# Kernel optimization log

Measured on AMD Instinct MI355X. Metric: run time of the kernel, lower is better.

The kernel has to match this reference:

```python
import jax, jax.numpy as jnp
import numpy as np

# Config constants (match init_kwargs / config)
B = 16        # config.BATCH_SIZE
T = 2048      # config.TRAIN_LEN
C = 256       # input channels (input_shape[-1])
K = 8         # kernel_size
F = 256       # nb_filters
DIL = 4       # dilation_rate


def setup_inputs() -> dict:
    key = jax.random.key(0)
    k1, k2, k3 = jax.random.split(key, 3)
    inputs = jax.random.normal(k1, (B, T, C), dtype=jnp.float32)
    kernel = jax.random.normal(k2, (C, K, F), dtype=jnp.float32) * 0.05
    bias = jax.random.normal(k3, (F,), dtype=jnp.float32) * 0.05
    return {"inputs": inputs, "kernel": kernel, "bias": bias}


def reference(inputs, kernel, bias):
    # Original TF layer computes, per (b,t,k,f):
    #   raw[b,t,k,f] = sum_c (x[b,t,c] * kernel[c,k,f] + bias[f])
    #               = conv[b,t,k,f] + C * bias[f]
    # (bias is added BEFORE the reduce_sum over the channel axis, so it is
    #  scaled by C — we reproduce that quirk faithfully.)
    # Then each (t,k) slice is scatter-added to output time t + k*dilation
    # (the gather_nd + zero-pad construction in TF implements exactly this
    #  dilated transposed-conv scatter; non-matching positions gather zeros),
    # and finally the last T timesteps are kept.
    Bq, Tq, Cq = inputs.shape
    Kq, Fq = kernel.shape[1], kernel.shape[2]
    conv = jnp.einsum('btc,ckf->btkf', inputs, kernel) + jnp.asarray(Cq, inputs.dtype) * bias
    L = Tq + (Kq - 1) * DIL  # final_time_len
    # scatter positions: out[i + j*DIL] += conv[:, i, j, :]
    pos = (jnp.arange(Tq)[:, None] + DIL * jnp.arange(Kq)[None, :]).reshape(-1)  # (T*K,)
    out = jnp.zeros((Bq, L, Fq), dtype=conv.dtype)
    out = out.at[:, pos, :].add(conv.reshape(Bq, Tq * Kq, Fq))
    return out[:, -Tq:, :]
```

## Files before the change

### kernel.cpp

```cpp
#include <hip/hip_runtime.h>
#include <hip/hip_bf16.h>


#define B_   16
#define T_   2048
#define C_   256
#define KT   8
#define F_   256
#define SH   28
#define BT   128
#define WIN  156
#define FB   19968
#define ABF  19968
#define ABFB 9984

typedef __attribute__((ext_vector_type(8))) short short8;
typedef __attribute__((ext_vector_type(4))) float floatx4;
typedef __attribute__((ext_vector_type(4))) int   intx4;

__device__ inline void gload16(const void* g, void* l) {
    __builtin_amdgcn_global_load_lds(
        (const __attribute__((address_space(1))) void*)g,
        (__attribute__((address_space(3))) void*)l, 16, 0, 0);
}

__device__ inline short8 cvt8(float4 a, float4 b) {
    float v[8] = {a.x, a.y, a.z, a.w, b.x, b.y, b.z, b.w};
    short8 r;
    #pragma unroll
    for (int i = 0; i < 8; ++i) {
        __hip_bfloat16 h = __float2bfloat16(v[i]);
        r[i] = *reinterpret_cast<const short*>(&h);
    }
    return r;
}

__global__ __launch_bounds__(256) void wprep_kernel(const float* __restrict__ W,
                                                    ushort* __restrict__ Wf) {
    const int tid  = threadIdx.x;
    const int fid  = blockIdx.x * 4 + (tid >> 6);
    const int lane = tid & 63;
    const int g    = fid & 15;
    const int S    = fid >> 4;
    const int j    = S & 7, c = S >> 3;
    const int c0   = c * 32 + (lane >> 4) * 8;
    const int f    = g * 16 + (lane & 15);
    short8 pk;
    #pragma unroll
    for (int i = 0; i < 8; ++i) {
        __hip_bfloat16 h = __float2bfloat16(W[((c0 + i) * KT + j) * F_ + f]);
        pk[i] = *reinterpret_cast<const short*>(&h);
    }
    *reinterpret_cast<short8*>(Wf + (size_t)fid * 512 + lane * 8) = pk;
}

__global__ __launch_bounds__(256, 2) void deconv_kernel(
        const float* __restrict__ x, const ushort* __restrict__ Wf,
        const float* __restrict__ bias, float* __restrict__ out) {
    __shared__ alignas(16) char smem[39936];
    const int bid = blockIdx.x;
    const int fh  = bid & 1;
    const int tb  = bid >> 1;
    const int b   = tb & 15;
    const int t0  = (tb >> 4) * BT;
    const int tid = threadIdx.x;
    const int w   = tid >> 6, lane = tid & 63;
    const int l16 = lane & 15, q = lane >> 4;
    const int wm  = w >> 1, wf2 = w & 1;
    const char* wfbase = (const char*)Wf +
        (size_t)(fh * 8 + wf2 * 4) * 1024 + (size_t)lane * 16;

#define VMW(N_) do { asm volatile("s_waitcnt vmcnt(" #N_ ")" ::: "memory"); \
        __builtin_amdgcn_sched_barrier(0); } while (0)
#define LKW() do { asm volatile("s_waitcnt lgkmcnt(0)" ::: "memory");       \
        __builtin_amdgcn_sched_barrier(0); } while (0)
#define BAR() do { __builtin_amdgcn_sched_barrier(0);                       \
        __builtin_amdgcn_s_barrier();                                       \
        asm volatile("" ::: "memory");                                      \
        __builtin_amdgcn_sched_barrier(0); } while (0)

#define A_ROUND(k_, cc_) do {                                               \
        const int u_ = (k_) * 256 + tid;                                    \
        if ((k_) < 4 || tid < 224) {                                        \
            const int row_ = u_ >> 3, s_ = u_ & 7;                          \
            const int v_   = (s_ + 8 - (row_ & 7)) & 7;                     \
            int tr_ = t0 + row_; if (tr_ > T_ - 1) tr_ = T_ - 1;            \
            gload16(x + ((size_t)(b * T_ + tr_) * C_ + (cc_) * 32 + v_ * 4),\
                    smem + ((k_) * 256 + w * 64) * 16);                     \
        } } while (0)

#define B_ISSUE(S_, sl_) do {                                               \
        const char* p_ = wfbase + (size_t)(S_) * 16384;                     \
        asm volatile("global_load_dwordx4 %0, %1, off"                      \
            : "=v"(bR[sl_][0]) : "v"(p_) : "memory");                       \
        asm volatile("global_load_dwordx4 %0, %1, off offset:1024"          \
            : "=v"(bR[sl_][1]) : "v"(p_) : "memory");                       \
        asm volatile("global_load_dwordx4 %0, %1, off offset:2048"          \
            : "=v"(bR[sl_][2]) : "v"(p_) : "memory");                       \
        asm volatile("global_load_dwordx4 %0, %1, off offset:3072"          \
            : "=v"(bR[sl_][3]) : "v"(p_) : "memory");                       \
        } while (0)

#define CVT_ROUND(r_, par_) do {                                            \
        if ((r_) < 2 || tid < 112) {                                        \
            const int task_ = (r_) * 256 + tid;                             \
            const int row_ = task_ >> 2, g_ = task_ & 3;                    \
            const int s1_ = (2 * g_ + row_) & 7;                            \
            const int s2_ = (2 * g_ + 1 + row_) & 7;                        \
            float4 u0_ = *(const float4*)(smem + (row_ * 8 + s1_) * 16);    \
            float4 u1_ = *(const float4*)(smem + (row_ * 8 + s2_) * 16);    \
            short8 pk_ = {0,0,0,0,0,0,0,0};                                 \
            if (t0 + row_ < T_) pk_ = cvt8(u0_, u1_);                       \
            const int p_ = g_ ^ ((row_ >> 1) & 3);                          \
            *(short8*)(smem + ABF + (par_) * ABFB + (row_ * 4 + p_) * 16)   \
                = pk_;                                                      \
        } } while (0)

#define LOAD_A(buf_, j_, arr) do {                                          \
        const char* ab_ = smem + ABF + (buf_) * ABFB;                       \
        _Pragma("unroll")                                                   \
        for (int mf = 0; mf < 4; ++mf) {                                    \
            const int row_ = wm * 64 + (SH - 4 * (j_)) + mf * 16 + l16;     \
            const int p_   = q ^ ((row_ >> 1) & 3);                         \
            arr[mf] = *(const short8*)(ab_ + (row_ * 4 + p_) * 16);         \
        } } while (0)

#define MFMA_TAP(arr, slot_) do {                                           \
        __builtin_amdgcn_s_setprio(1);                                      \
        _Pragma("unroll")                                                   \
        for (int mf = 0; mf < 4; ++mf)                                      \
            _Pragma("unroll")                                               \
            for (int nf = 0; nf < 4; ++nf)                                  \
                acc[mf][nf] = __builtin_amdgcn_mfma_f32_16x16x32_bf16(      \
                    arr[mf], *(short8*)&bR[slot_][nf],                      \
                    acc[mf][nf], 0, 0, 0);                                  \
        __builtin_amdgcn_s_setprio(0);                                      \
        } while (0)

#define CHUNK(c_) do {                                                      \
        LOAD_A((c_) & 1, 0, a0);                                            \
        A_ROUND(0, (c_)+1); A_ROUND(1, (c_)+1); A_ROUND(2, (c_)+1);         \
        A_ROUND(3, (c_)+1); A_ROUND(4, (c_)+1);                             \
        LOAD_A((c_) & 1, 1, a1);                                            \
        B_ISSUE((c_)*8+2, (((c_)*8+2)%3)); VMW(13);                         \
        MFMA_TAP(a0, (((c_)*8+0)%3));                                       \
        LOAD_A((c_) & 1, 2, a0);                                            \
        B_ISSUE((c_)*8+3, (((c_)*8+3)%3)); VMW(13);                         \
        MFMA_TAP(a1, (((c_)*8+1)%3));                                       \
        LOAD_A((c_) & 1, 3, a1);                                            \
        B_ISSUE((c_)*8+4, (((c_)*8+4)%3)); VMW(8);                          \
        MFMA_TAP(a0, (((c_)*8+2)%3));                                       \
        BAR();                                                              \
        LOAD_A((c_) & 1, 4, a0);                                            \
        B_ISSUE((c_)*8+5, (((c_)*8+5)%3)); VMW(8);                          \
        MFMA_TAP(a1, (((c_)*8+3)%3));                                       \
        LOAD_A((c_) & 1, 5, a1);                                            \
        CVT_ROUND(0, ((c_)+1)&1);                                           \
        B_ISSUE((c_)*8+6, (((c_)*8+6)%3)); VMW(8);                          \
        MFMA_TAP(a0, (((c_)*8+4)%3));                                       \
        LOAD_A((c_) & 1, 6, a0);                                            \
        CVT_ROUND(1, ((c_)+1)&1);                                           \
        B_ISSUE((c_)*8+7, (((c_)*8+7)%3)); VMW(8);                          \
        MFMA_TAP(a1, (((c_)*8+5)%3));                                       \
        LOAD_A((c_) & 1, 7, a1);                                            \
        CVT_ROUND(2, ((c_)+1)&1);                                           \
        B_ISSUE((c_)*8+8, (((c_)*8+8)%3)); VMW(8);                          \
        MFMA_TAP(a0, (((c_)*8+6)%3));                                       \
        B_ISSUE((c_)*8+9, (((c_)*8+9)%3)); VMW(8);                          \
        MFMA_TAP(a1, (((c_)*8+7)%3));                                       \
        LKW(); BAR();                                                       \
        } while (0)

    float bf4[4];
    #pragma unroll
    for (int nf = 0; nf < 4; ++nf)
        bf4[nf] = bias[fh * 128 + wf2 * 64 + nf * 16 + l16];

    floatx4 acc[4][4];
    #pragma unroll
    for (int mf = 0; mf < 4; ++mf)
        #pragma unroll
        for (int nf = 0; nf < 4; ++nf)
            acc[mf][nf] = (floatx4){0.f, 0.f, 0.f, 0.f};

    short8 a0[4], a1[4];
    intx4  bR[3][4];

    A_ROUND(0, 0); A_ROUND(1, 0); A_ROUND(2, 0); A_ROUND(3, 0); A_ROUND(4, 0);
    B_ISSUE(0, 0); B_ISSUE(1, 1);
    VMW(8);
    BAR();
    CVT_ROUND(0, 0); CVT_ROUND(1, 0); CVT_ROUND(2, 0);
    LKW(); BAR();

    CHUNK(0); CHUNK(1); CHUNK(2); CHUNK(3);
    CHUNK(4); CHUNK(5); CHUNK(6);

    LOAD_A(1, 0, a0);
    LOAD_A(1, 1, a1);
    B_ISSUE(58, 1); VMW(8); MFMA_TAP(a0, 2); LOAD_A(1, 2, a0);
    B_ISSUE(59, 2); VMW(8); MFMA_TAP(a1, 0); LOAD_A(1, 3, a1);
    B_ISSUE(60, 0); VMW(8); MFMA_TAP(a0, 1); LOAD_A(1, 4, a0);
    B_ISSUE(61, 1); VMW(8); MFMA_TAP(a1, 2); LOAD_A(1, 5, a1);
    B_ISSUE(62, 2); VMW(8); MFMA_TAP(a0, 0); LOAD_A(1, 6, a0);
    B_ISSUE(63, 0); VMW(8); MFMA_TAP(a1, 1); LOAD_A(1, 7, a1);
    VMW(4); MFMA_TAP(a0, 2);
    VMW(0); MFMA_TAP(a1, 0);

    #pragma unroll
    for (int mf = 0; mf < 4; ++mf) {
        #pragma unroll
        for (int nf = 0; nf < 4; ++nf) {
            const int f = fh * 128 + wf2 * 64 + nf * 16 + l16;
            #pragma unroll
            for (int r = 0; r < 4; ++r) {
                const int t = t0 + wm * 64 + mf * 16 + q * 4 + r;
                const int jmin = (t < T_ - SH) ? 0 : (((t - (T_ - SH)) >> 2) + 1);
                out[(size_t)(b * T_ + t) * F_ + f] =
                    acc[mf][nf][r] + (float)(8 - jmin) * 256.0f * bf4[nf];
            }
        }
    }
#undef VMW
#undef LKW
#undef BAR
#undef A_ROUND
#undef B_ISSUE
#undef CVT_ROUND
#undef LOAD_A
#undef MFMA_TAP
#undef CHUNK
}

extern "C" void kernel_launch(void* const* d_in, const int* in_sizes, int n_in,
                              void* d_out, int out_size, void* d_ws, size_t ws_size,
                              hipStream_t stream) {
    const float* x    = (const float*)d_in[0];
    const float* W    = (const float*)d_in[1];
    const float* bias = (const float*)d_in[2];
    float* out = (float*)d_out;
    ushort* Wf = (ushort*)d_ws;

    wprep_kernel<<<256, 256, 0, stream>>>(W, Wf);
    deconv_kernel<<<512, 256, 0, stream>>>(x, Wf, bias, out);
}
```

Measured before the change: 43.89 us.

## Halve time tile to 64 rows and regrid warps over filters only

Shrinks the per-block time tile from 128 to 64 rows and reassigns the four waves to split only the filter dimension, each wave now covering 32 filters instead of 64. The grid doubles to 1024 blocks, smaller LDS and register footprints allow four blocks per CU, and the A staging, conversion rounds, B loads and wait counts are rescaled to match. The aim is better CU fill and latency hiding on a machine with many CUs. In exchange each block re-reads a larger halo fraction of x and more weight traffic per output, which lowers arithmetic intensity.

After: 51.55 us. 1.17x slower.

```diff
diff --git a/kernel.cpp b/kernel.cpp
--- a/kernel.cpp
+++ b/kernel.cpp
@@ -8,11 +8,11 @@
 #define KT   8
 #define F_   256
 #define SH   28
-#define BT   128
-#define WIN  156
-#define FB   19968
-#define ABF  19968
-#define ABFB 9984
+#define BT   64
+#define WIN  92
+#define FB   11776
+#define ABF  11776
+#define ABFB 5888
 
 typedef __attribute__((ext_vector_type(8))) short short8;
 typedef __attribute__((ext_vector_type(4))) float floatx4;
@@ -54,21 +54,20 @@
     *reinterpret_cast<short8*>(Wf + (size_t)fid * 512 + lane * 8) = pk;
 }
 
-__global__ __launch_bounds__(256, 2) void deconv_kernel(
+__global__ __launch_bounds__(256, 4) void deconv_kernel(
         const float* __restrict__ x, const ushort* __restrict__ Wf,
         const float* __restrict__ bias, float* __restrict__ out) {
-    __shared__ alignas(16) char smem[39936];
+    __shared__ alignas(16) char smem[23552];
     const int bid = blockIdx.x;
     const int fh  = bid & 1;
     const int tb  = bid >> 1;
     const int b   = tb & 15;
     const int t0  = (tb >> 4) * BT;
     const int tid = threadIdx.x;
-    const int w   = tid >> 6, lane = tid & 63;
+    const int wf  = tid >> 6, lane = tid & 63;
     const int l16 = lane & 15, q = lane >> 4;
-    const int wm  = w >> 1, wf2 = w & 1;
     const char* wfbase = (const char*)Wf +
-        (size_t)(fh * 8 + wf2 * 4) * 1024 + (size_t)lane * 16;
+        (size_t)(fh * 8 + wf * 2) * 1024 + (size_t)lane * 16;
 
 #define VMW(N_) do { asm volatile("s_waitcnt vmcnt(" #N_ ")" ::: "memory"); \
         __builtin_amdgcn_sched_barrier(0); } while (0)
@@ -81,12 +80,12 @@
 
 #define A_ROUND(k_, cc_) do {                                               \
         const int u_ = (k_) * 256 + tid;                                    \
-        if ((k_) < 4 || tid < 224) {                                        \
+        if ((k_) < 2 || tid < 224) {                                        \
             const int row_ = u_ >> 3, s_ = u_ & 7;                          \
             const int v_   = (s_ + 8 - (row_ & 7)) & 7;                     \
             int tr_ = t0 + row_; if (tr_ > T_ - 1) tr_ = T_ - 1;            \
             gload16(x + ((size_t)(b * T_ + tr_) * C_ + (cc_) * 32 + v_ * 4),\
-                    smem + ((k_) * 256 + w * 64) * 16);                     \
+                    smem + ((k_) * 256 + wf * 64) * 16);                    \
         } } while (0)
 
 #define B_ISSUE(S_, sl_) do {                                               \
@@ -95,14 +94,10 @@
             : "=v"(bR[sl_][0]) : "v"(p_) : "memory");                       \
         asm volatile("global_load_dwordx4 %0, %1, off offset:1024"          \
             : "=v"(bR[sl_][1]) : "v"(p_) : "memory");                       \
-        asm volatile("global_load_dwordx4 %0, %1, off offset:2048"          \
-            : "=v"(bR[sl_][2]) : "v"(p_) : "memory");                       \
-        asm volatile("global_load_dwordx4 %0, %1, off offset:3072"          \
-            : "=v"(bR[sl_][3]) : "v"(p_) : "memory");                       \
         } while (0)
 
 #define CVT_ROUND(r_, par_) do {                                            \
-        if ((r_) < 2 || tid < 112) {                                        \
+        if ((r_) < 1 || tid < 112) {                                        \
             const int task_ = (r_) * 256 + tid;                             \
             const int row_ = task_ >> 2, g_ = task_ & 3;                    \
             const int s1_ = (2 * g_ + row_) & 7;                            \
@@ -120,7 +115,7 @@
         const char* ab_ = smem + ABF + (buf_) * ABFB;                       \
         _Pragma("unroll")                                                   \
         for (int mf = 0; mf < 4; ++mf) {                                    \
-            const int row_ = wm * 64 + (SH - 4 * (j_)) + mf * 16 + l16;     \
+            const int row_ = (SH - 4 * (j_)) + mf * 16 + l16;               \
             const int p_   = q ^ ((row_ >> 1) & 3);                         \
             arr[mf] = *(const short8*)(ab_ + (row_ * 4 + p_) * 16);         \
         } } while (0)
@@ -130,7 +125,7 @@
         _Pragma("unroll")                                                   \
         for (int mf = 0; mf < 4; ++mf)                                      \
             _Pragma("unroll")                                               \
-            for (int nf = 0; nf < 4; ++nf)                                  \
+            for (int nf = 0; nf < 2; ++nf)                                  \
                 acc[mf][nf] = __builtin_amdgcn_mfma_f32_16x16x32_bf16(      \
                     arr[mf], *(short8*)&bR[slot_][nf],                      \
                     acc[mf][nf], 0, 0, 0);                                  \
@@ -140,57 +135,54 @@
 #define CHUNK(c_) do {                                                      \
         LOAD_A((c_) & 1, 0, a0);                                            \
         A_ROUND(0, (c_)+1); A_ROUND(1, (c_)+1); A_ROUND(2, (c_)+1);         \
-        A_ROUND(3, (c_)+1); A_ROUND(4, (c_)+1);                             \
         LOAD_A((c_) & 1, 1, a1);                                            \
-        B_ISSUE((c_)*8+2, (((c_)*8+2)%3)); VMW(13);                         \
+        B_ISSUE((c_)*8+2, (((c_)*8+2)%3)); VMW(7);                          \
         MFMA_TAP(a0, (((c_)*8+0)%3));                                       \
         LOAD_A((c_) & 1, 2, a0);                                            \
-        B_ISSUE((c_)*8+3, (((c_)*8+3)%3)); VMW(13);                         \
+        B_ISSUE((c_)*8+3, (((c_)*8+3)%3)); VMW(7);                          \
         MFMA_TAP(a1, (((c_)*8+1)%3));                                       \
         LOAD_A((c_) & 1, 3, a1);                                            \
-        B_ISSUE((c_)*8+4, (((c_)*8+4)%3)); VMW(8);                          \
+        B_ISSUE((c_)*8+4, (((c_)*8+4)%3)); VMW(4);                          \
+        BAR();                                                              \
         MFMA_TAP(a0, (((c_)*8+2)%3));                                       \
-        BAR();                                                              \
         LOAD_A((c_) & 1, 4, a0);                                            \
-        B_ISSUE((c_)*8+5, (((c_)*8+5)%3)); VMW(8);                          \
+        B_ISSUE((c_)*8+5, (((c_)*8+5)%3)); VMW(4);                          \
         MFMA_TAP(a1, (((c_)*8+3)%3));                                       \
         LOAD_A((c_) & 1, 5, a1);                                            \
         CVT_ROUND(0, ((c_)+1)&1);                                           \
-        B_ISSUE((c_)*8+6, (((c_)*8+6)%3)); VMW(8);                          \
+        B_ISSUE((c_)*8+6, (((c_)*8+6)%3)); VMW(4);                          \
         MFMA_TAP(a0, (((c_)*8+4)%3));                                       \
         LOAD_A((c_) & 1, 6, a0);                                            \
         CVT_ROUND(1, ((c_)+1)&1);                                           \
-        B_ISSUE((c_)*8+7, (((c_)*8+7)%3)); VMW(8);                          \
+        B_ISSUE((c_)*8+7, (((c_)*8+7)%3)); VMW(4);                          \
         MFMA_TAP(a1, (((c_)*8+5)%3));                                       \
         LOAD_A((c_) & 1, 7, a1);                                            \
-        CVT_ROUND(2, ((c_)+1)&1);                                           \
-        B_ISSUE((c_)*8+8, (((c_)*8+8)%3)); VMW(8);                          \
+        B_ISSUE((c_)*8+8, (((c_)*8+8)%3)); VMW(4);                          \
         MFMA_TAP(a0, (((c_)*8+6)%3));                                       \
-        B_ISSUE((c_)*8+9, (((c_)*8+9)%3)); VMW(8);                          \
+        B_ISSUE((c_)*8+9, (((c_)*8+9)%3)); VMW(4);                          \
         MFMA_TAP(a1, (((c_)*8+7)%3));                                       \
         LKW(); BAR();                                                       \
         } while (0)
 
-    float bf4[4];
-    #pragma unroll
-    for (int nf = 0; nf < 4; ++nf)
-        bf4[nf] = bias[fh * 128 + wf2 * 64 + nf * 16 + l16];
-
-    floatx4 acc[4][4];
-    #pragma unroll
-    for (int mf = 0; mf < 4; ++mf)
-        #pragma unroll
-        for (int nf = 0; nf < 4; ++nf)
-            acc[mf][nf] = (floatx4){0.f, 0.f, 0.f, 0.f};
+    float bf2[2];
+    bf2[0] = bias[fh * 128 + wf * 32 + l16];
+    bf2[1] = bias[fh * 128 + wf * 32 + 16 + l16];
+
+    floatx4 acc[4][2];
+    #pragma unroll
+    for (int mf = 0; mf < 4; ++mf) {
+        acc[mf][0] = (floatx4){0.f, 0.f, 0.f, 0.f};
+        acc[mf][1] = (floatx4){0.f, 0.f, 0.f, 0.f};
+    }
 
     short8 a0[4], a1[4];
-    intx4  bR[3][4];
-
-    A_ROUND(0, 0); A_ROUND(1, 0); A_ROUND(2, 0); A_ROUND(3, 0); A_ROUND(4, 0);
+    intx4  bR[3][2];
+
+    A_ROUND(0, 0); A_ROUND(1, 0); A_ROUND(2, 0);
     B_ISSUE(0, 0); B_ISSUE(1, 1);
-    VMW(8);
+    VMW(4);
     BAR();
-    CVT_ROUND(0, 0); CVT_ROUND(1, 0); CVT_ROUND(2, 0);
+    CVT_ROUND(0, 0); CVT_ROUND(1, 0);
     LKW(); BAR();
 
     CHUNK(0); CHUNK(1); CHUNK(2); CHUNK(3);
@@ -198,26 +190,26 @@
 
     LOAD_A(1, 0, a0);
     LOAD_A(1, 1, a1);
-    B_ISSUE(58, 1); VMW(8); MFMA_TAP(a0, 2); LOAD_A(1, 2, a0);
-    B_ISSUE(59, 2); VMW(8); MFMA_TAP(a1, 0); LOAD_A(1, 3, a1);
-    B_ISSUE(60, 0); VMW(8); MFMA_TAP(a0, 1); LOAD_A(1, 4, a0);
-    B_ISSUE(61, 1); VMW(8); MFMA_TAP(a1, 2); LOAD_A(1, 5, a1);
-    B_ISSUE(62, 2); VMW(8); MFMA_TAP(a0, 0); LOAD_A(1, 6, a0);
-    B_ISSUE(63, 0); VMW(8); MFMA_TAP(a1, 1); LOAD_A(1, 7, a1);
-    VMW(4); MFMA_TAP(a0, 2);
+    B_ISSUE(58, 1); VMW(4); MFMA_TAP(a0, 2); LOAD_A(1, 2, a0);
+    B_ISSUE(59, 2); VMW(4); MFMA_TAP(a1, 0); LOAD_A(1, 3, a1);
+    B_ISSUE(60, 0); VMW(4); MFMA_TAP(a0, 1); LOAD_A(1, 4, a0);
+    B_ISSUE(61, 1); VMW(4); MFMA_TAP(a1, 2); LOAD_A(1, 5, a1);
+    B_ISSUE(62, 2); VMW(4); MFMA_TAP(a0, 0); LOAD_A(1, 6, a0);
+    B_ISSUE(63, 0); VMW(4); MFMA_TAP(a1, 1); LOAD_A(1, 7, a1);
+    VMW(2); MFMA_TAP(a0, 2);
     VMW(0); MFMA_TAP(a1, 0);
 
     #pragma unroll
     for (int mf = 0; mf < 4; ++mf) {
         #pragma unroll
-        for (int nf = 0; nf < 4; ++nf) {
-            const int f = fh * 128 + wf2 * 64 + nf * 16 + l16;
+        for (int nf = 0; nf < 2; ++nf) {
+            const int f = fh * 128 + wf * 32 + nf * 16 + l16;
             #pragma unroll
             for (int r = 0; r < 4; ++r) {
-                const int t = t0 + wm * 64 + mf * 16 + q * 4 + r;
+                const int t = t0 + mf * 16 + q * 4 + r;
                 const int jmin = (t < T_ - SH) ? 0 : (((t - (T_ - SH)) >> 2) + 1);
                 out[(size_t)(b * T_ + t) * F_ + f] =
-                    acc[mf][nf][r] + (float)(8 - jmin) * 256.0f * bf4[nf];
+                    acc[mf][nf][r] + (float)(8 - jmin) * 256.0f * bf2[nf];
             }
         }
     }
@@ -242,5 +234,5 @@
     ushort* Wf = (ushort*)d_ws;
 
     wprep_kernel<<<256, 256, 0, stream>>>(W, Wf);
-    deconv_kernel<<<512, 256, 0, stream>>>(x, Wf, bias, out);
-}
+    deconv_kernel<<<1024, 256, 0, stream>>>(x, Wf, bias, out);
+}
```

## Add producer wavefront to load and convert activations, specializing compute warps

Applied to the files above, without the earlier changes.

Splits the block into four MFMA compute waves and a fifth producer wave. The producer loads fp32 activations into registers, converts them to bf16, and writes them into a double-buffered LDS tile. Compute waves no longer issue the global-to-LDS loads or do the conversion rounds. This drops the fp32 staging buffer and shrinks LDS, so the launch bound asks for 3 blocks per CU. The risk is that a single producer wave with many outstanding loads and a full vmcnt(0) wait per stage becomes the bottleneck, and the barrier handshake each chunk must stay correctly matched between the two roles.

New measurement: 44.47 us. About the same (+1.3%).

```diff
diff --git a/kernel.cpp b/kernel.cpp
--- a/kernel.cpp
+++ b/kernel.cpp
@@ -9,31 +9,11 @@
 #define F_   256
 #define SH   28
 #define BT   128
-#define WIN  156
-#define FB   19968
-#define ABF  19968
 #define ABFB 9984
 
 typedef __attribute__((ext_vector_type(8))) short short8;
 typedef __attribute__((ext_vector_type(4))) float floatx4;
 typedef __attribute__((ext_vector_type(4))) int   intx4;
-
-__device__ inline void gload16(const void* g, void* l) {
-    __builtin_amdgcn_global_load_lds(
-        (const __attribute__((address_space(1))) void*)g,
-        (__attribute__((address_space(3))) void*)l, 16, 0, 0);
-}
-
-__device__ inline short8 cvt8(float4 a, float4 b) {
-    float v[8] = {a.x, a.y, a.z, a.w, b.x, b.y, b.z, b.w};
-    short8 r;
-    #pragma unroll
-    for (int i = 0; i < 8; ++i) {
-        __hip_bfloat16 h = __float2bfloat16(v[i]);
-        r[i] = *reinterpret_cast<const short*>(&h);
-    }
-    return r;
-}
 
 __global__ __launch_bounds__(256) void wprep_kernel(const float* __restrict__ W,
                                                     ushort* __restrict__ Wf) {
@@ -54,10 +34,25 @@
     *reinterpret_cast<short8*>(Wf + (size_t)fid * 512 + lane * 8) = pk;
 }
 
-__global__ __launch_bounds__(256, 2) void deconv_kernel(
+__device__ inline short8 cvt8v(floatx4 a, floatx4 b) {
+    short8 r;
+    #pragma unroll
+    for (int i = 0; i < 4; ++i) {
+        __hip_bfloat16 h = __float2bfloat16(a[i]);
+        r[i] = *reinterpret_cast<const short*>(&h);
+    }
+    #pragma unroll
+    for (int i = 0; i < 4; ++i) {
+        __hip_bfloat16 h = __float2bfloat16(b[i]);
+        r[i + 4] = *reinterpret_cast<const short*>(&h);
+    }
+    return r;
+}
+
+__global__ __launch_bounds__(320, 3) void deconv_kernel(
         const float* __restrict__ x, const ushort* __restrict__ Wf,
         const float* __restrict__ bias, float* __restrict__ out) {
-    __shared__ alignas(16) char smem[39936];
+    __shared__ alignas(16) char smem[2 * ABFB];
     const int bid = blockIdx.x;
     const int fh  = bid & 1;
     const int tb  = bid >> 1;
@@ -66,28 +61,19 @@
     const int tid = threadIdx.x;
     const int w   = tid >> 6, lane = tid & 63;
     const int l16 = lane & 15, q = lane >> 4;
-    const int wm  = w >> 1, wf2 = w & 1;
-    const char* wfbase = (const char*)Wf +
-        (size_t)(fh * 8 + wf2 * 4) * 1024 + (size_t)lane * 16;
 
 #define VMW(N_) do { asm volatile("s_waitcnt vmcnt(" #N_ ")" ::: "memory"); \
         __builtin_amdgcn_sched_barrier(0); } while (0)
 #define LKW() do { asm volatile("s_waitcnt lgkmcnt(0)" ::: "memory");       \
         __builtin_amdgcn_sched_barrier(0); } while (0)
 #define BAR() do { __builtin_amdgcn_sched_barrier(0);                       \
-        __builtin_amdgcn_s_barrier();                                       \
-        asm volatile("" ::: "memory");                                      \
+        asm volatile("s_barrier" ::: "memory");                             \
         __builtin_amdgcn_sched_barrier(0); } while (0)
 
-#define A_ROUND(k_, cc_) do {                                               \
-        const int u_ = (k_) * 256 + tid;                                    \
-        if ((k_) < 4 || tid < 224) {                                        \
-            const int row_ = u_ >> 3, s_ = u_ & 7;                          \
-            const int v_   = (s_ + 8 - (row_ & 7)) & 7;                     \
-            int tr_ = t0 + row_; if (tr_ > T_ - 1) tr_ = T_ - 1;            \
-            gload16(x + ((size_t)(b * T_ + tr_) * C_ + (cc_) * 32 + v_ * 4),\
-                    smem + ((k_) * 256 + w * 64) * 16);                     \
-        } } while (0)
+    if (w < 4) {
+        const int wm = w >> 1, wf2 = w & 1;
+        const char* wfbase = (const char*)Wf +
+            (size_t)(fh * 8 + wf2 * 4) * 1024 + (size_t)lane * 16;
 
 #define B_ISSUE(S_, sl_) do {                                               \
         const char* p_ = wfbase + (size_t)(S_) * 16384;                     \
@@ -101,23 +87,8 @@
             : "=v"(bR[sl_][3]) : "v"(p_) : "memory");                       \
         } while (0)
 
-#define CVT_ROUND(r_, par_) do {                                            \
-        if ((r_) < 2 || tid < 112) {                                        \
-            const int task_ = (r_) * 256 + tid;                             \
-            const int row_ = task_ >> 2, g_ = task_ & 3;                    \
-            const int s1_ = (2 * g_ + row_) & 7;                            \
-            const int s2_ = (2 * g_ + 1 + row_) & 7;                        \
-            float4 u0_ = *(const float4*)(smem + (row_ * 8 + s1_) * 16);    \
-            float4 u1_ = *(const float4*)(smem + (row_ * 8 + s2_) * 16);    \
-            short8 pk_ = {0,0,0,0,0,0,0,0};                                 \
-            if (t0 + row_ < T_) pk_ = cvt8(u0_, u1_);                       \
-            const int p_ = g_ ^ ((row_ >> 1) & 3);                          \
-            *(short8*)(smem + ABF + (par_) * ABFB + (row_ * 4 + p_) * 16)   \
-                = pk_;                                                      \
-        } } while (0)
-
 #define LOAD_A(buf_, j_, arr) do {                                          \
-        const char* ab_ = smem + ABF + (buf_) * ABFB;                       \
+        const char* ab_ = smem + (buf_) * ABFB;                             \
         _Pragma("unroll")                                                   \
         for (int mf = 0; mf < 4; ++mf) {                                    \
             const int row_ = wm * 64 + (SH - 4 * (j_)) + mf * 16 + l16;     \
@@ -137,99 +108,128 @@
         __builtin_amdgcn_s_setprio(0);                                      \
         } while (0)
 
-#define CHUNK(c_) do {                                                      \
-        LOAD_A((c_) & 1, 0, a0);                                            \
-        A_ROUND(0, (c_)+1); A_ROUND(1, (c_)+1); A_ROUND(2, (c_)+1);         \
-        A_ROUND(3, (c_)+1); A_ROUND(4, (c_)+1);                             \
-        LOAD_A((c_) & 1, 1, a1);                                            \
-        B_ISSUE((c_)*8+2, (((c_)*8+2)%3)); VMW(13);                         \
-        MFMA_TAP(a0, (((c_)*8+0)%3));                                       \
-        LOAD_A((c_) & 1, 2, a0);                                            \
-        B_ISSUE((c_)*8+3, (((c_)*8+3)%3)); VMW(13);                         \
-        MFMA_TAP(a1, (((c_)*8+1)%3));                                       \
-        LOAD_A((c_) & 1, 3, a1);                                            \
-        B_ISSUE((c_)*8+4, (((c_)*8+4)%3)); VMW(8);                          \
-        MFMA_TAP(a0, (((c_)*8+2)%3));                                       \
+#define CTAP(c_, t_, arr)                                                   \
+        B_ISSUE((c_)*8+(t_)+2, (((c_)*8+(t_)+2)%3)); VMW(8);                \
+        MFMA_TAP(arr, (((c_)*8+(t_))%3));                                   \
+        if ((t_) < 6) LOAD_A((c_) & 1, (t_) + 2, arr);
+
+#define CCHUNK(c_) do {                                                     \
+        LOAD_A((c_) & 1, 0, a0); LOAD_A((c_) & 1, 1, a1);                   \
+        CTAP(c_, 0, a0) CTAP(c_, 1, a1)                                     \
+        CTAP(c_, 2, a0) CTAP(c_, 3, a1)                                     \
+        CTAP(c_, 4, a0) CTAP(c_, 5, a1)                                     \
+        CTAP(c_, 6, a0) CTAP(c_, 7, a1)                                     \
         BAR();                                                              \
-        LOAD_A((c_) & 1, 4, a0);                                            \
-        B_ISSUE((c_)*8+5, (((c_)*8+5)%3)); VMW(8);                          \
-        MFMA_TAP(a1, (((c_)*8+3)%3));                                       \
-        LOAD_A((c_) & 1, 5, a1);                                            \
-        CVT_ROUND(0, ((c_)+1)&1);                                           \
-        B_ISSUE((c_)*8+6, (((c_)*8+6)%3)); VMW(8);                          \
-        MFMA_TAP(a0, (((c_)*8+4)%3));                                       \
-        LOAD_A((c_) & 1, 6, a0);                                            \
-        CVT_ROUND(1, ((c_)+1)&1);                                           \
-        B_ISSUE((c_)*8+7, (((c_)*8+7)%3)); VMW(8);                          \
-        MFMA_TAP(a1, (((c_)*8+5)%3));                                       \
-        LOAD_A((c_) & 1, 7, a1);                                            \
-        CVT_ROUND(2, ((c_)+1)&1);                                           \
-        B_ISSUE((c_)*8+8, (((c_)*8+8)%3)); VMW(8);                          \
-        MFMA_TAP(a0, (((c_)*8+6)%3));                                       \
-        B_ISSUE((c_)*8+9, (((c_)*8+9)%3)); VMW(8);                          \
-        MFMA_TAP(a1, (((c_)*8+7)%3));                                       \
-        LKW(); BAR();                                                       \
-        } while (0)
-
-    float bf4[4];
-    #pragma unroll
-    for (int nf = 0; nf < 4; ++nf)
-        bf4[nf] = bias[fh * 128 + wf2 * 64 + nf * 16 + l16];
-
-    floatx4 acc[4][4];
-    #pragma unroll
-    for (int mf = 0; mf < 4; ++mf)
+        } while (0)
+
+        float bf4[4];
         #pragma unroll
         for (int nf = 0; nf < 4; ++nf)
-            acc[mf][nf] = (floatx4){0.f, 0.f, 0.f, 0.f};
-
-    short8 a0[4], a1[4];
-    intx4  bR[3][4];
-
-    A_ROUND(0, 0); A_ROUND(1, 0); A_ROUND(2, 0); A_ROUND(3, 0); A_ROUND(4, 0);
-    B_ISSUE(0, 0); B_ISSUE(1, 1);
-    VMW(8);
-    BAR();
-    CVT_ROUND(0, 0); CVT_ROUND(1, 0); CVT_ROUND(2, 0);
-    LKW(); BAR();
-
-    CHUNK(0); CHUNK(1); CHUNK(2); CHUNK(3);
-    CHUNK(4); CHUNK(5); CHUNK(6);
-
-    LOAD_A(1, 0, a0);
-    LOAD_A(1, 1, a1);
-    B_ISSUE(58, 1); VMW(8); MFMA_TAP(a0, 2); LOAD_A(1, 2, a0);
-    B_ISSUE(59, 2); VMW(8); MFMA_TAP(a1, 0); LOAD_A(1, 3, a1);
-    B_ISSUE(60, 0); VMW(8); MFMA_TAP(a0, 1); LOAD_A(1, 4, a0);
-    B_ISSUE(61, 1); VMW(8); MFMA_TAP(a1, 2); LOAD_A(1, 5, a1);
-    B_ISSUE(62, 2); VMW(8); MFMA_TAP(a0, 0); LOAD_A(1, 6, a0);
-    B_ISSUE(63, 0); VMW(8); MFMA_TAP(a1, 1); LOAD_A(1, 7, a1);
-    VMW(4); MFMA_TAP(a0, 2);
-    VMW(0); MFMA_TAP(a1, 0);
-
-    #pragma unroll
-    for (int mf = 0; mf < 4; ++mf) {
+            bf4[nf] = bias[fh * 128 + wf2 * 64 + nf * 16 + l16];
+
+        floatx4 acc[4][4];
         #pragma unroll
-        for (int nf = 0; nf < 4; ++nf) {
-            const int f = fh * 128 + wf2 * 64 + nf * 16 + l16;
+        for (int mf = 0; mf < 4; ++mf)
             #pragma unroll
-            for (int r = 0; r < 4; ++r) {
-                const int t = t0 + wm * 64 + mf * 16 + q * 4 + r;
-                const int jmin = (t < T_ - SH) ? 0 : (((t - (T_ - SH)) >> 2) + 1);
-                out[(size_t)(b * T_ + t) * F_ + f] =
-                    acc[mf][nf][r] + (float)(8 - jmin) * 256.0f * bf4[nf];
+            for (int nf = 0; nf < 4; ++nf)
+                acc[mf][nf] = (floatx4){0.f, 0.f, 0.f, 0.f};
+
+        short8 a0[4], a1[4];
+        intx4  bR[3][4];
+
+        VMW(0);
+        B_ISSUE(0, 0); B_ISSUE(1, 1);
+        BAR();
+
+        CCHUNK(0); CCHUNK(1); CCHUNK(2); CCHUNK(3);
+        CCHUNK(4); CCHUNK(5); CCHUNK(6);
+
+        {
+            LOAD_A(1, 0, a0); LOAD_A(1, 1, a1);
+            B_ISSUE(58, 1); VMW(8); MFMA_TAP(a0, 2); LOAD_A(1, 2, a0);
+            B_ISSUE(59, 2); VMW(8); MFMA_TAP(a1, 0); LOAD_A(1, 3, a1);
+            B_ISSUE(60, 0); VMW(8); MFMA_TAP(a0, 1); LOAD_A(1, 4, a0);
+            B_ISSUE(61, 1); VMW(8); MFMA_TAP(a1, 2); LOAD_A(1, 5, a1);
+            B_ISSUE(62, 2); VMW(8); MFMA_TAP(a0, 0); LOAD_A(1, 6, a0);
+            B_ISSUE(63, 0); VMW(8); MFMA_TAP(a1, 1); LOAD_A(1, 7, a1);
+            VMW(4); MFMA_TAP(a0, 2);
+            VMW(0); MFMA_TAP(a1, 0);
+        }
+
+        #pragma unroll
+        for (int mf = 0; mf < 4; ++mf) {
+            #pragma unroll
+            for (int nf = 0; nf < 4; ++nf) {
+                const int f = fh * 128 + wf2 * 64 + nf * 16 + l16;
+                #pragma unroll
+                for (int r = 0; r < 4; ++r) {
+                    const int t = t0 + wm * 64 + mf * 16 + q * 4 + r;
+                    const int jmin =
+                        (t < T_ - SH) ? 0 : (((t - (T_ - SH)) >> 2) + 1);
+                    out[(size_t)(b * T_ + t) * F_ + f] =
+                        acc[mf][nf][r] + (float)(8 - jmin) * 256.0f * bf4[nf];
+                }
             }
         }
+#undef B_ISSUE
+#undef LOAD_A
+#undef MFMA_TAP
+#undef CTAP
+#undef CCHUNK
+    } else {
+        floatx4 ps[10][2];
+
+#define PROD_LOAD(r_, cs_) do {                                             \
+        const int u_ = (r_) * 64 + lane;                                    \
+        const int row_ = u_ >> 2, pp_ = u_ & 3;                             \
+        const int g_ = pp_ ^ ((row_ >> 1) & 3);                             \
+        int tr_ = t0 + row_; if (tr_ > T_ - 1) tr_ = T_ - 1;                \
+        const char* p_ = (const char*)(x +                                  \
+            ((size_t)(b * T_ + tr_) * C_ + (cs_) * 32 + g_ * 8));           \
+        asm volatile("global_load_dwordx4 %0, %1, off"                      \
+            : "=v"(ps[r_][0]) : "v"(p_) : "memory");                        \
+        asm volatile("global_load_dwordx4 %0, %1, off offset:16"            \
+            : "=v"(ps[r_][1]) : "v"(p_) : "memory");                        \
+        } while (0)
+
+#define PROD_WRITE(r_, buf_) do {                                           \
+        const int u_ = (r_) * 64 + lane;                                    \
+        const int row_ = u_ >> 2, pp_ = u_ & 3;                             \
+        if ((r_) < 9 || row_ < 156) {                                       \
+            short8 pk_ = {0,0,0,0,0,0,0,0};                                 \
+            if (t0 + row_ < T_) pk_ = cvt8v(ps[r_][0], ps[r_][1]);          \
+            *(short8*)(smem + (buf_) * ABFB + (row_ * 4 + pp_) * 16) = pk_; \
+        } } while (0)
+
+#define PROD_STAGE(cs_, buf_) do {                                          \
+        PROD_LOAD(0, cs_); PROD_LOAD(1, cs_); PROD_LOAD(2, cs_);            \
+        PROD_LOAD(3, cs_); PROD_LOAD(4, cs_); PROD_LOAD(5, cs_);            \
+        PROD_LOAD(6, cs_); PROD_LOAD(7, cs_); PROD_LOAD(8, cs_);            \
+        PROD_LOAD(9, cs_);                                                  \
+        VMW(0);                                                             \
+        PROD_WRITE(0, buf_); PROD_WRITE(1, buf_); PROD_WRITE(2, buf_);      \
+        PROD_WRITE(3, buf_); PROD_WRITE(4, buf_); PROD_WRITE(5, buf_);      \
+        PROD_WRITE(6, buf_); PROD_WRITE(7, buf_); PROD_WRITE(8, buf_);      \
+        PROD_WRITE(9, buf_);                                                \
+        LKW();                                                              \
+        } while (0)
+
+        PROD_STAGE(0, 0);
+        BAR();
+        PROD_STAGE(1, 1); BAR();
+        PROD_STAGE(2, 0); BAR();
+        PROD_STAGE(3, 1); BAR();
+        PROD_STAGE(4, 0); BAR();
+        PROD_STAGE(5, 1); BAR();
+        PROD_STAGE(6, 0); BAR();
+        PROD_STAGE(7, 1); BAR();
+#undef PROD_LOAD
+#undef PROD_WRITE
+#undef PROD_STAGE
     }
 #undef VMW
 #undef LKW
 #undef BAR
-#undef A_ROUND
-#undef B_ISSUE
-#undef CVT_ROUND
-#undef LOAD_A
-#undef MFMA_TAP
-#undef CHUNK
 }
 
 extern "C" void kernel_launch(void* const* d_in, const int* in_sizes, int n_in,
@@ -242,5 +242,5 @@
     ushort* Wf = (ushort*)d_ws;
 
     wprep_kernel<<<256, 256, 0, stream>>>(W, Wf);
-    deconv_kernel<<<512, 256, 0, stream>>>(x, Wf, bias, out);
-}
+    deconv_kernel<<<512, 320, 0, stream>>>(x, Wf, bias, out);
+}
```

## Switch deconv GEMM from 16x16x32 to 32x32x16 bf16 MFMA tiles

Applied to the files above, without the earlier changes.

Changes the per-wave MFMA tiling from a 4x4 grid of 16x16x32 instructions to a 2x2 grid of 32x32x16 instructions, each issued twice per K=32 step. The weight prepack, the LDS A-fragment layout, and the epilogue row mapping are reworked to match the 32x32 operand and accumulator layouts. Larger MFMA tiles cut operand fetch per FLOP and instruction count. The occupancy hint of 2 blocks per SM is also dropped from launch bounds. The epilogue now writes 16 rows per lane with a more complex row mapping.

After: 48.65 us. 1.11x slower.

```diff
diff --git a/kernel.cpp b/kernel.cpp
--- a/kernel.cpp
+++ b/kernel.cpp
@@ -16,6 +16,7 @@
 
 typedef __attribute__((ext_vector_type(8))) short short8;
 typedef __attribute__((ext_vector_type(4))) float floatx4;
+typedef __attribute__((ext_vector_type(16))) float floatx16;
 typedef __attribute__((ext_vector_type(4))) int   intx4;
 
 __device__ inline void gload16(const void* g, void* l) {
@@ -40,21 +41,23 @@
     const int tid  = threadIdx.x;
     const int fid  = blockIdx.x * 4 + (tid >> 6);
     const int lane = tid & 63;
-    const int g    = fid & 15;
-    const int S    = fid >> 4;
-    const int j    = S & 7, c = S >> 3;
-    const int c0   = c * 32 + (lane >> 4) * 8;
-    const int f    = g * 16 + (lane & 15);
+    const int l5 = lane & 31, h = lane >> 5;
+    const int knf = fid & 3, kh = knf >> 1, nf = knf & 1;
+    const int fqg = (fid >> 2) & 3;
+    const int S   = fid >> 4;
+    const int j   = S & 7, ch = S >> 3;
+    const int c0  = ch * 32 + kh * 16 + h * 8;
+    const int f   = fqg * 64 + nf * 32 + l5;
     short8 pk;
     #pragma unroll
     for (int i = 0; i < 8; ++i) {
-        __hip_bfloat16 h = __float2bfloat16(W[((c0 + i) * KT + j) * F_ + f]);
-        pk[i] = *reinterpret_cast<const short*>(&h);
+        __hip_bfloat16 v = __float2bfloat16(W[((c0 + i) * KT + j) * F_ + f]);
+        pk[i] = *reinterpret_cast<const short*>(&v);
     }
     *reinterpret_cast<short8*>(Wf + (size_t)fid * 512 + lane * 8) = pk;
 }
 
-__global__ __launch_bounds__(256, 2) void deconv_kernel(
+__global__ __launch_bounds__(256) void deconv_kernel(
         const float* __restrict__ x, const ushort* __restrict__ Wf,
         const float* __restrict__ bias, float* __restrict__ out) {
     __shared__ alignas(16) char smem[39936];
@@ -65,10 +68,10 @@
     const int t0  = (tb >> 4) * BT;
     const int tid = threadIdx.x;
     const int w   = tid >> 6, lane = tid & 63;
-    const int l16 = lane & 15, q = lane >> 4;
-    const int wm  = w >> 1, wf2 = w & 1;
+    const int l5  = lane & 31, h = lane >> 5;
+    const int wm  = w >> 1, fq2 = w & 1;
     const char* wfbase = (const char*)Wf +
-        (size_t)(fh * 8 + wf2 * 4) * 1024 + (size_t)lane * 16;
+        (size_t)(fh * 2 + fq2) * 4096 + (size_t)lane * 16;
 
 #define VMW(N_) do { asm volatile("s_waitcnt vmcnt(" #N_ ")" ::: "memory"); \
         __builtin_amdgcn_sched_barrier(0); } while (0)
@@ -119,21 +122,28 @@
 #define LOAD_A(buf_, j_, arr) do {                                          \
         const char* ab_ = smem + ABF + (buf_) * ABFB;                       \
         _Pragma("unroll")                                                   \
-        for (int mf = 0; mf < 4; ++mf) {                                    \
-            const int row_ = wm * 64 + (SH - 4 * (j_)) + mf * 16 + l16;     \
-            const int p_   = q ^ ((row_ >> 1) & 3);                         \
-            arr[mf] = *(const short8*)(ab_ + (row_ * 4 + p_) * 16);         \
-        } } while (0)
+        for (int kh = 0; kh < 2; ++kh)                                      \
+            _Pragma("unroll")                                               \
+            for (int mf = 0; mf < 2; ++mf) {                                \
+                const int row_ = wm * 64 + (SH - 4 * (j_)) + mf * 32 + l5;  \
+                const int p_ = (kh * 2 + h) ^ ((row_ >> 1) & 3);            \
+                arr[kh * 2 + mf] = *(const short8*)(ab_ + (row_ * 4 + p_)   \
+                                                    * 16);                  \
+            } } while (0)
 
 #define MFMA_TAP(arr, slot_) do {                                           \
         __builtin_amdgcn_s_setprio(1);                                      \
         _Pragma("unroll")                                                   \
-        for (int mf = 0; mf < 4; ++mf)                                      \
+        for (int mf = 0; mf < 2; ++mf)                                      \
             _Pragma("unroll")                                               \
-            for (int nf = 0; nf < 4; ++nf)                                  \
-                acc[mf][nf] = __builtin_amdgcn_mfma_f32_16x16x32_bf16(      \
-                    arr[mf], *(short8*)&bR[slot_][nf],                      \
+            for (int nf = 0; nf < 2; ++nf) {                                \
+                acc[mf][nf] = __builtin_amdgcn_mfma_f32_32x32x16_bf16(      \
+                    arr[0 * 2 + mf], *(short8*)&bR[slot_][0 * 2 + nf],      \
                     acc[mf][nf], 0, 0, 0);                                  \
+                acc[mf][nf] = __builtin_amdgcn_mfma_f32_32x32x16_bf16(      \
+                    arr[1 * 2 + mf], *(short8*)&bR[slot_][1 * 2 + nf],      \
+                    acc[mf][nf], 0, 0, 0);                                  \
+            }                                                               \
         __builtin_amdgcn_s_setprio(0);                                      \
         } while (0)
 
@@ -171,17 +181,17 @@
         LKW(); BAR();                                                       \
         } while (0)
 
-    float bf4[4];
-    #pragma unroll
-    for (int nf = 0; nf < 4; ++nf)
-        bf4[nf] = bias[fh * 128 + wf2 * 64 + nf * 16 + l16];
-
-    floatx4 acc[4][4];
-    #pragma unroll
-    for (int mf = 0; mf < 4; ++mf)
+    float bf2[2];
+    bf2[0] = bias[fh * 128 + fq2 * 64 + l5];
+    bf2[1] = bias[fh * 128 + fq2 * 64 + 32 + l5];
+
+    floatx16 acc[2][2];
+    #pragma unroll
+    for (int mf = 0; mf < 2; ++mf)
         #pragma unroll
-        for (int nf = 0; nf < 4; ++nf)
-            acc[mf][nf] = (floatx4){0.f, 0.f, 0.f, 0.f};
+        for (int nf = 0; nf < 2; ++nf)
+            #pragma unroll
+            for (int r = 0; r < 16; ++r) acc[mf][nf][r] = 0.f;
 
     short8 a0[4], a1[4];
     intx4  bR[3][4];
@@ -208,16 +218,17 @@
     VMW(0); MFMA_TAP(a1, 0);
 
     #pragma unroll
-    for (int mf = 0; mf < 4; ++mf) {
+    for (int mf = 0; mf < 2; ++mf) {
         #pragma unroll
-        for (int nf = 0; nf < 4; ++nf) {
-            const int f = fh * 128 + wf2 * 64 + nf * 16 + l16;
+        for (int nf = 0; nf < 2; ++nf) {
+            const int f = fh * 128 + fq2 * 64 + nf * 32 + l5;
             #pragma unroll
-            for (int r = 0; r < 4; ++r) {
-                const int t = t0 + wm * 64 + mf * 16 + q * 4 + r;
+            for (int r = 0; r < 16; ++r) {
+                const int rowin = (r & 3) + 8 * (r >> 2) + 4 * h;
+                const int t = t0 + wm * 64 + mf * 32 + rowin;
                 const int jmin = (t < T_ - SH) ? 0 : (((t - (T_ - SH)) >> 2) + 1);
                 out[(size_t)(b * T_ + t) * F_ + f] =
-                    acc[mf][nf][r] + (float)(8 - jmin) * 256.0f * bf4[nf];
+                    acc[mf][nf][r] + (float)(8 - jmin) * 256.0f * bf2[nf];
             }
         }
     }
```
